# Kernel optimization log

Hardware: AMD Instinct MI355X
Metric: run time of the kernel (lower is better)

Reference implementation:

```python
import jax, jax.numpy as jnp
import numpy as np

B, CIN, CMID, COUT, H, W = 4, 64, 128, 128, 128, 128
K = 9  # 3x3 taps
EPS = 1e-5


def conv3x3(x, w, b):
    # standard 3x3 conv, stride 1, pad 1, NCHW / OIHW
    y = jax.lax.conv_general_dilated(x, w, (1, 1), ((1, 1), (1, 1)),
                                     dimension_numbers=('NCHW', 'OIHW', 'NCHW'))
    return y + b[None, :, None, None]


def deform_conv3x3(x, offset, w, b):
    # torchvision DeformConv2d semantics (v1, no mask), kernel 3, pad 1, stride 1.
    # offset: [B, 2*K, H, W] with per-tap (dy, dx) pairs.
    Bn, C, Hn, Wn = x.shape
    off = offset.reshape(Bn, K, 2, Hn, Wn)
    off_y, off_x = off[:, :, 0], off[:, :, 1]          # [B,K,H,W]
    ky = (jnp.arange(K) // 3).astype(x.dtype)          # tap row 0..2
    kx = (jnp.arange(K) % 3).astype(x.dtype)           # tap col 0..2
    # sampling positions: p = out_pos - pad + tap + offset
    py = jnp.arange(Hn, dtype=x.dtype)[None, None, :, None] - 1.0 + ky[None, :, None, None] + off_y
    px = jnp.arange(Wn, dtype=x.dtype)[None, None, None, :] - 1.0 + kx[None, :, None, None] + off_x
    y0 = jnp.floor(py); x0 = jnp.floor(px)
    wy1 = py - y0; wx1 = px - x0                       # bilinear fractions
    y0i = y0.astype(jnp.int32); x0i = x0.astype(jnp.int32)
    xf = x.reshape(Bn, C, Hn * Wn)

    def gather(iy, ix):
        valid = ((iy >= 0) & (iy < Hn) & (ix >= 0) & (ix < Wn)).astype(x.dtype)
        idx = jnp.clip(iy, 0, Hn - 1) * Wn + jnp.clip(ix, 0, Wn - 1)  # [B,K,H,W]
        g = jax.vmap(lambda xb, ib: xb[:, ib])(xf, idx)               # [B,C,K,H,W]
        return g, valid

    g00, v00 = gather(y0i, x0i)
    g01, v01 = gather(y0i, x0i + 1)
    g10, v10 = gather(y0i + 1, x0i)
    g11, v11 = gather(y0i + 1, x0i + 1)

    def wmul(g, v, wgt):
        return g * (v * wgt)[:, None]                  # broadcast over channel dim

    sampled = (wmul(g00, v00, (1 - wy1) * (1 - wx1)) +
               wmul(g01, v01, (1 - wy1) * wx1) +
               wmul(g10, v10, wy1 * (1 - wx1)) +
               wmul(g11, v11, wy1 * wx1))              # [B,C,K,H,W]
    out = jnp.einsum('bckhw,ock->bohw', sampled, w.reshape(w.shape[0], C, K))
    return out + b[None, :, None, None]


def batchnorm_relu(x, gamma, beta):
    # training-mode BN: batch statistics over (N,H,W), biased variance
    mean = jnp.mean(x, axis=(0, 2, 3), keepdims=True)
    var = jnp.mean(jnp.square(x - mean), axis=(0, 2, 3), keepdims=True)
    y = (x - mean) * jax.lax.rsqrt(var + EPS)
    return jax.nn.relu(y * gamma[None, :, None, None] + beta[None, :, None, None])


def setup_inputs() -> dict:
    key = jax.random.key(0)
    ks = jax.random.split(key, 13)
    s = 0.05  # small weights keep offsets small / sampling mostly in-bounds
    return {
        'x': jax.random.normal(ks[0], (B, CIN, H, W), jnp.float32),
        'w_off1': jax.random.normal(ks[1], (2 * K, CIN, 3, 3), jnp.float32) * s,
        'b_off1': jnp.zeros((2 * K,), jnp.float32),
        'w1': jax.random.normal(ks[2], (CMID, CIN, 3, 3), jnp.float32) * s,
        'b1': jax.random.normal(ks[3], (CMID,), jnp.float32) * s,
        'g1': jnp.ones((CMID,), jnp.float32),
        'be1': jnp.zeros((CMID,), jnp.float32),
        'w_off2': jax.random.normal(ks[4], (2 * K, CMID, 3, 3), jnp.float32) * s,
        'b_off2': jnp.zeros((2 * K,), jnp.float32),
        'w2': jax.random.normal(ks[5], (COUT, CMID, 3, 3), jnp.float32) * s,
        'b2': jax.random.normal(ks[6], (COUT,), jnp.float32) * s,
        'g2': jnp.ones((COUT,), jnp.float32),
        'be2': jnp.zeros((COUT,), jnp.float32),
    }


def reference(x, w_off1, b_off1, w1, b1, g1, be1, w_off2, b_off2, w2, b2, g2, be2):
    offset1 = conv3x3(x, w_off1, b_off1)
    out = deform_conv3x3(x, offset1, w1, b1)
    out = batchnorm_relu(out, g1, be1)
    offset2 = conv3x3(out, w_off2, b_off2)
    out = deform_conv3x3(out, offset2, w2, b2)
    out = batchnorm_relu(out, g2, be2)
    return out
```

## Files before the change

kernel.cpp:

```cpp
#include <hip/hip_runtime.h>
#include <hip/hip_bf16.h>

#define BB 4
#define H_ 128
#define W_ 128
#define HWP 16384
#define KOFF 18

typedef short short8 __attribute__((ext_vector_type(8)));
typedef float floatx4 __attribute__((ext_vector_type(4)));

#define WS_AB   16
#define WS_CVT  288
#define CVT_TOTAL 4447396
#define WS_WF1  4447744
#define WS_WF2  4484608
#define WS_XT   4558336
#define WS_Y1   7835136
#define WS_Y1T  16223744
#define WS_XTL  18320896
#define WS_WFO1 20418048
#define WS_WFO2 20436480
#define WS_PART 21600000
#define WS_Y2   WS_Y1

#define R_X     0
#define R_WOFF1 4194304
#define R_BOFF1 4204672
#define R_W1    4204690
#define R_B1    4278418
#define R_G1    4278546
#define R_BE1   4278674
#define R_WOFF2 4278802
#define R_BOFF2 4299538
#define R_W2    4299556
#define R_B2    4447012
#define R_G2    4447140
#define R_BE2   4447268

struct SrcPtrs { const void* p[13]; };

__device__ inline short f2bf(float f) {
    __hip_bfloat16 h = __float2bfloat16(f);
    return *reinterpret_cast<short*>(&h);
}
__device__ inline float bf2f(unsigned short u) {
    return __uint_as_float(((unsigned int)u) << 16);
}
__device__ inline float bfu_lo(unsigned int u) { return __uint_as_float(u << 16); }
__device__ inline float bfu_hi(unsigned int u) { return __uint_as_float(u & 0xFFFF0000u); }
__device__ inline float rl_f(float v, int i) {
    return __int_as_float(__builtin_amdgcn_readlane(__float_as_int(v), i));
}

__global__ void probe_dtype_k(const unsigned int* __restrict__ g1, int* __restrict__ flag) {
    if (threadIdx.x == 0 && blockIdx.x == 0) {
        flag[0] = ((g1[0] & 0xFFFFu) != 0u) ? 1 : 0;
    }
}

__global__ __launch_bounds__(256) void convert_inputs_k(SrcPtrs sp, float* __restrict__ dst,
                                                        const int* __restrict__ flag, int total) {
    int i = blockIdx.x * 256 + threadIdx.x;
    if (i >= total) return;
    constexpr int prefix[13] = {0, R_WOFF1, R_BOFF1, R_W1, R_B1, R_G1, R_BE1,
                                R_WOFF2, R_BOFF2, R_W2, R_B2, R_G2, R_BE2};
    const void* src = sp.p[0];
    int base = 0;
#pragma unroll
    for (int q = 1; q < 13; ++q) {
        if (i >= prefix[q]) { src = sp.p[q]; base = prefix[q]; }
    }
    int local = i - base;
    float v;
    if (flag[0] != 0) {
        v = bf2f(((const unsigned short*)src)[local]);
    } else {
        v = ((const float*)src)[local];
    }
    dst[i] = v;
}

template <int CIN>
__global__ __launch_bounds__(256) void wf_build_k(const float* __restrict__ w, short* __restrict__ wf) {
    constexpr int KSTEPS = CIN * 9 / 32;
    int idx = blockIdx.x * 256 + threadIdx.x;
    int j    = idx & 7;
    int lane = (idx >> 3) & 63;
    int rem  = idx >> 9;
    int ks   = rem % KSTEPS;
    int ct   = rem / KSTEPS;
    int co = ct * 16 + (lane & 15);
    int k  = ks * 32 + (lane >> 4) * 8 + j;
    int ci = k & (CIN - 1);
    int kk = k / CIN;
    wf[idx] = f2bf(w[(co * CIN + ci) * 9 + kk]);
}

template <int CIN>
__global__ __launch_bounds__(256) void wf_off_build_k(const float* __restrict__ w, short* __restrict__ wf) {
    constexpr int KSTEPS = CIN * 9 / 32;
    int idx = blockIdx.x * 256 + threadIdx.x;
    int j    = idx & 7;
    int lane = (idx >> 3) & 63;
    int rem  = idx >> 9;
    int ks   = rem % KSTEPS;
    int cc   = rem / KSTEPS;
    int sel  = cc >> 1;
    int co = (cc & 1) * 16 + (lane & 15);
    int k  = ks * 32 + (lane >> 4) * 8 + j;
    int ci = k & (CIN - 1);
    int kk = k / CIN;
    float v = (co < KOFF) ? w[(co * CIN + ci) * 9 + kk] : 0.f;
    short hi = f2bf(v);
    wf[idx] = sel ? f2bf(v - bf2f((unsigned short)hi)) : hi;
}

__global__ __launch_bounds__(256) void xt_build_k(const float* __restrict__ x,
                                                  unsigned short* __restrict__ xt,
                                                  unsigned short* __restrict__ xtl) {
    __shared__ __align__(4) short s_t[64 * 66];
    __shared__ __align__(4) short s_tl[64 * 66];
    int bi  = blockIdx.x;
    int hw0 = (bi & 255) * 64;
    int b   = bi >> 8;
    int t   = threadIdx.x;
    int hwp = t & 63;
#pragma unroll
    for (int it = 0; it < 16; ++it) {
        int c = it * 4 + (t >> 6);
        float v = x[((long)(b * 64 + c) << 14) + hw0 + hwp];
        short hi = f2bf(v);
        s_t[hwp * 66 + c]  = hi;
        s_tl[hwp * 66 + c] = f2bf(v - bf2f((unsigned short)hi));
    }
    __syncthreads();
#pragma unroll
    for (int it = 0; it < 8; ++it) {
        int i  = it * 256 + t;
        int c2 = (i & 31) * 2;
        int hw2 = i >> 5;
        long da = ((long)((b << 14) + hw0 + hw2)) * 64 + c2;
        *(int*)&xt[da]  = *(const int*)&s_t[hw2 * 66 + c2];
        *(int*)&xtl[da] = *(const int*)&s_tl[hw2 * 66 + c2];
    }
}

__device__ inline int conv_tpk(int h, int w0, int lane, int wv) {
    int tpk = 0;
    if (lane < 36) {
        int r = wv + 8 * lane;
        int p = r & 31;
        int k = r >> 5;
        int y = h - 1 + k / 3;
        int x = w0 + p - 1 + (k % 3);
        int valid = (y >= 0 && y < H_ && x >= 0 && x < W_) ? 1 : 0;
        int yc = min(max(y, 0), H_ - 1), xc = min(max(x, 0), W_ - 1);
        tpk = (yc * W_ + xc) | (valid << 16);
    }
    return tpk;
}

template <int NJ>
__device__ inline void conv_load64(const unsigned short* __restrict__ xb, unsigned int* ub,
                                   int half, int li, int tpk, int J0) {
#pragma unroll
    for (int j = 0; j < NJ; ++j) {
        int jj = J0 + j;
        int pkA = __builtin_amdgcn_readlane(tpk, 2 * jj);
        int pkB = __builtin_amdgcn_readlane(tpk, 2 * jj + 1);
        int pk = half ? pkB : pkA;
        unsigned int u = *(const unsigned int*)(xb + (pk & 0xFFFF) * 64 + 2 * li);
        ub[j] = (pk >> 16) ? u : 0u;
    }
}
template <int NJ, int PADc>
__device__ inline void conv_store64(short* __restrict__ s_samp, const unsigned int* ub,
                                    int half, int li, int wv, int J0) {
#pragma unroll
    for (int j = 0; j < NJ; ++j) {
        int jj = J0 + j;
        int r = wv + 8 * (half ? (2 * jj + 1) : (2 * jj));
        *(unsigned int*)&s_samp[(r & 31) * PADc + (r >> 5) * 64 + 2 * li] = ub[j];
    }
}
template <int I0, int NJ>
__device__ inline void conv_load128(const unsigned short* __restrict__ xb, unsigned int* ub,
                                    int lane, int tpk) {
#pragma unroll
    for (int j = 0; j < NJ; ++j) {
        int pk = __builtin_amdgcn_readlane(tpk, I0 + j);
        unsigned int u = *(const unsigned int*)(xb + (pk & 0xFFFF) * 128 + 2 * lane);
        ub[j] = (pk >> 16) ? u : 0u;
    }
}
template <int I0, int NJ, int KKB, int PADc>
__device__ inline void conv_store128(short* __restrict__ s_samp, const unsigned int* ub,
                                     int wv, int lane) {
#pragma unroll
    for (int j = 0; j < NJ; ++j) {
        int r = wv + 8 * (I0 + j);
        *(unsigned int*)&s_samp[(r & 31) * PADc + ((r >> 5) - KKB) * 128 + 2 * lane] = ub[j];
    }
}

__device__ inline void build_table2_lds(const float* __restrict__ s_off,
                                        int h, int w0, int lane, int wv,
                                        int& tpk, float& tw0, float& tw1, float& tw2, float& tw3) {
    tpk = 0; tw0 = tw1 = tw2 = tw3 = 0.f;
    if (lane < 36) {
        int r = wv + 8 * lane;
        int p = r & 31;
        int k = r >> 5;
        int wpix = w0 + p;
        float oy = s_off[(2 * k) * 32 + p];
        float ox = s_off[(2 * k + 1) * 32 + p];
        float py = (float)(h - 1 + (k / 3)) + oy;
        float px = (float)(wpix - 1 + (k % 3)) + ox;
        float fy = floorf(py), fx = floorf(px);
        float wy = py - fy, wx = px - fx;
        int y0 = (int)fy, x0 = (int)fx;
        int y1 = y0 + 1, x1 = x0 + 1;
        bool vy0 = (y0 >= 0) && (y0 < H_);
        bool vy1 = (y1 >= 0) && (y1 < H_);
        bool vx0 = (x0 >= 0) && (x0 < W_);
        bool vx1 = (x1 >= 0) && (x1 < W_);
        float wy0 = 1.f - wy, wx0 = 1.f - wx;
        tw0 = (vy0 && vx0) ? wy0 * wx0 : 0.f;
        tw1 = (vy0 && vx1) ? wy0 * wx  : 0.f;
        tw2 = (vy1 && vx0) ? wy  * wx0 : 0.f;
        tw3 = (vy1 && vx1) ? wy  * wx  : 0.f;
        int iy0 = min(max(y0, 0), H_ - 1), iy1 = min(max(y1, 0), H_ - 1);
        int ix0 = min(max(x0, 0), W_ - 1), ix1 = min(max(x1, 0), W_ - 1);
        int dx = ix1 - ix0;
        int dy = iy1 - iy0;
        tpk = (iy0 * W_ + ix0) | (dx << 14) | (dy << 15);
    }
}

template <int NB>
__device__ inline void gather_batch128v2(const unsigned short* __restrict__ xb, short* __restrict__ s_samp,
                                         int i0, int kkbase, int wv, int lane,
                                         int tpk, float tw0, float tw1, float tw2, float tw3) {
    constexpr int PADc = 648;
    uint4 ub[NB];
#pragma unroll
    for (int j = 0; j < NB; ++j) {
        int pk = __builtin_amdgcn_readlane(tpk, i0 + j);
        const unsigned short* b00 = xb + (pk & 0x3FFF) * 128;
        const unsigned short* b01 = b00 + ((pk >> 14) & 1) * 128;
        const unsigned short* b10 = b00 + ((pk >> 15) & 1) * (W_ * 128);
        const unsigned short* b11 = b01 + ((pk >> 15) & 1) * (W_ * 128);
        ub[j].x = *(const unsigned int*)(b00 + 2 * lane);
        ub[j].y = *(const unsigned int*)(b01 + 2 * lane);
        ub[j].z = *(const unsigned int*)(b10 + 2 * lane);
        ub[j].w = *(const unsigned int*)(b11 + 2 * lane);
    }
#pragma unroll
    for (int j = 0; j < NB; ++j) {
        int i = i0 + j;
        int r = wv + 8 * i;
        float w00 = rl_f(tw0, i), w01 = rl_f(tw1, i), w10 = rl_f(tw2, i), w11 = rl_f(tw3, i);
        float vlo = w00 * bfu_lo(ub[j].x) + w01 * bfu_lo(ub[j].y)
                  + w10 * bfu_lo(ub[j].z) + w11 * bfu_lo(ub[j].w);
        float vhi = w00 * bfu_hi(ub[j].x) + w01 * bfu_hi(ub[j].y)
                  + w10 * bfu_hi(ub[j].z) + w11 * bfu_hi(ub[j].w);
        __hip_bfloat162 h2 = __float22bfloat162_rn(make_float2(vlo, vhi));
        *(unsigned int*)&s_samp[(r & 31) * PADc + ((r >> 5) - kkbase) * 128 + 2 * lane] =
            *reinterpret_cast<unsigned int*>(&h2);
    }
}

template <int NBP>
__device__ inline void gather_batch64v2(const unsigned short* __restrict__ xb, short* __restrict__ s_samp,
                                        int i0, int wv, int half, int li,
                                        int tpk, float tw0, float tw1, float tw2, float tw3) {
    constexpr int PADc = 584;
    uint4 ub[NBP];
#pragma unroll
    for (int j = 0; j < NBP; ++j) {
        int iA = i0 + 2 * j, iB = iA + 1;
        int pkA = __builtin_amdgcn_readlane(tpk, iA);
        int pkB = __builtin_amdgcn_readlane(tpk, iB);
        int pk = half ? pkB : pkA;
        const unsigned short* b00 = xb + (pk & 0x3FFF) * 64;
        const unsigned short* b01 = b00 + ((pk >> 14) & 1) * 64;
        const unsigned short* b10 = b00 + ((pk >> 15) & 1) * (W_ * 64);
        const unsigned short* b11 = b01 + ((pk >> 15) & 1) * (W_ * 64);
        ub[j].x = *(const unsigned int*)(b00 + 2 * li);
        ub[j].y = *(const unsigned int*)(b01 + 2 * li);
        ub[j].z = *(const unsigned int*)(b10 + 2 * li);
        ub[j].w = *(const unsigned int*)(b11 + 2 * li);
    }
#pragma unroll
    for (int j = 0; j < NBP; ++j) {
        int iA = i0 + 2 * j, iB = iA + 1;
        float w00 = half ? rl_f(tw0, iB) : rl_f(tw0, iA);
        float w01 = half ? rl_f(tw1, iB) : rl_f(tw1, iA);
        float w10 = half ? rl_f(tw2, iB) : rl_f(tw2, iA);
        float w11 = half ? rl_f(tw3, iB) : rl_f(tw3, iA);
        float vlo = w00 * bfu_lo(ub[j].x) + w01 * bfu_lo(ub[j].y)
                  + w10 * bfu_lo(ub[j].z) + w11 * bfu_lo(ub[j].w);
        float vhi = w00 * bfu_hi(ub[j].x) + w01 * bfu_hi(ub[j].y)
                  + w10 * bfu_hi(ub[j].z) + w11 * bfu_hi(ub[j].w);
        __hip_bfloat162 h2 = __float22bfloat162_rn(make_float2(vlo, vhi));
        int r = wv + 8 * (half ? iB : iA);
        *(unsigned int*)&s_samp[(r & 31) * PADc + (r >> 5) * 64 + 2 * li] =
            *reinterpret_cast<unsigned int*>(&h2);
    }
}

__global__ __launch_bounds__(512, 4) void fused64_k(const unsigned short* __restrict__ xt,
                                                    const unsigned short* __restrict__ xtl,
                                                    const short* __restrict__ wfo,
                                                    const float* __restrict__ boff,
                                                    const short* __restrict__ wf,
                                                    const float* __restrict__ bias,
                                                    float* __restrict__ out) {
    constexpr int KSTEPS = 18;
    constexpr int PADc = 584;
    __shared__ __align__(16) short s_samp[32 * PADc];
    __shared__ float s_off[KOFF * 32];
    float* s_redf = (float*)s_samp;

    int bi = blockIdx.x;
    int w0 = (bi & 3) * 32;
    int h  = (bi >> 2) & 127;
    int b  = bi >> 9;
    int t  = threadIdx.x;
    int lane = t & 63;
    int wv   = t >> 6;

    const unsigned short* xbh = xt  + (long)b * HWP * 64;
    const unsigned short* xbl = xtl + (long)b * HWP * 64;
    int half = lane >> 5, li = lane & 31;
    int p_   = lane & 15;
    int quad = lane >> 4;

    {
        int tpkc = conv_tpk(h, w0, lane, wv);
        int ct  = wv & 1;
        int ksl = wv >> 1;
        floatx4 acc0, acc1;
#pragma unroll
        for (int r = 0; r < 4; ++r) {
            int co = ct * 16 + quad * 4 + r;
            float bv = (ksl == 0 && co < KOFF) ? boff[co] : 0.f;
            acc0[r] = bv;
            acc1[r] = bv;
        }

        {
            unsigned int ubA[16];
            conv_load64<16>(xbh, ubA, half, li, tpkc, 0);
            conv_store64<16, PADc>(s_samp, ubA, half, li, wv, 0);
        }
        __syncthreads();
        unsigned int ubC[2];
        conv_load64<2>(xbh, ubC, half, li, tpkc, 16);
#pragma unroll
        for (int ki = 0; ki < 4; ++ki) {
            int ks = ksl * 4 + ki;
            short8 b0 = *(const short8*)&s_samp[p_ * PADc + ks * 32 + quad * 8];
            short8 b1 = *(const short8*)&s_samp[(16 + p_) * PADc + ks * 32 + quad * 8];
            short8 ah = *(const short8*)&wfo[(((long)ct * KSTEPS + ks) * 64 + lane) * 8];
            short8 al = *(const short8*)&wfo[(((long)(2 + ct) * KSTEPS + ks) * 64 + lane) * 8];
            acc0 = __builtin_amdgcn_mfma_f32_16x16x32_bf16(ah, b0, acc0, 0, 0, 0);
            acc0 = __builtin_amdgcn_mfma_f32_16x16x32_bf16(al, b0, acc0, 0, 0, 0);
            acc1 = __builtin_amdgcn_mfma_f32_16x16x32_bf16(ah, b1, acc1, 0, 0, 0);
            acc1 = __builtin_amdgcn_mfma_f32_16x16x32_bf16(al, b1, acc1, 0, 0, 0);
        }
        __syncthreads();
        conv_store64<2, PADc>(s_samp, ubC, half, li, wv, 16);
        __syncthreads();
        unsigned int ubA2[16];
        conv_load64<16>(xbl, ubA2, half, li, tpkc, 0);
        if (ksl < 2) {
            int ks = 16 + ksl;
            short8 b0 = *(const short8*)&s_samp[p_ * PADc + ks * 32 + quad * 8];
            short8 b1 = *(const short8*)&s_samp[(16 + p_) * PADc + ks * 32 + quad * 8];
            short8 ah = *(const short8*)&wfo[(((long)ct * KSTEPS + ks) * 64 + lane) * 8];
            short8 al = *(const short8*)&wfo[(((long)(2 + ct) * KSTEPS + ks) * 64 + lane) * 8];
            acc0 = __builtin_amdgcn_mfma_f32_16x16x32_bf16(ah, b0, acc0, 0, 0, 0);
            acc0 = __builtin_amdgcn_mfma_f32_16x16x32_bf16(al, b0, acc0, 0, 0, 0);
            acc1 = __builtin_amdgcn_mfma_f32_16x16x32_bf16(ah, b1, acc1, 0, 0, 0);
            acc1 = __builtin_amdgcn_mfma_f32_16x16x32_bf16(al, b1, acc1, 0, 0, 0);
        }
        __syncthreads();
        conv_store64<16, PADc>(s_samp, ubA2, half, li, wv, 0);
        __syncthreads();
        conv_load64<2>(xbl, ubC, half, li, tpkc, 16);
#pragma unroll
        for (int ki = 0; ki < 4; ++ki) {
            int ks = ksl * 4 + ki;
            short8 b0 = *(const short8*)&s_samp[p_ * PADc + ks * 32 + quad * 8];
            short8 b1 = *(const short8*)&s_samp[(16 + p_) * PADc + ks * 32 + quad * 8];
            short8 ah = *(const short8*)&wfo[(((long)ct * KSTEPS + ks) * 64 + lane) * 8];
            acc0 = __builtin_amdgcn_mfma_f32_16x16x32_bf16(ah, b0, acc0, 0, 0, 0);
            acc1 = __builtin_amdgcn_mfma_f32_16x16x32_bf16(ah, b1, acc1, 0, 0, 0);
        }
        __syncthreads();
        conv_store64<2, PADc>(s_samp, ubC, half, li, wv, 16);
        __syncthreads();
        if (ksl < 2) {
            int ks = 16 + ksl;
            short8 b0 = *(const short8*)&s_samp[p_ * PADc + ks * 32 + quad * 8];
            short8 b1 = *(const short8*)&s_samp[(16 + p_) * PADc + ks * 32 + quad * 8];
            short8 ah = *(const short8*)&wfo[(((long)ct * KSTEPS + ks) * 64 + lane) * 8];
            acc0 = __builtin_amdgcn_mfma_f32_16x16x32_bf16(ah, b0, acc0, 0, 0, 0);
            acc1 = __builtin_amdgcn_mfma_f32_16x16x32_bf16(ah, b1, acc1, 0, 0, 0);
        }

        __syncthreads();
        if (ksl != 0) {
#pragma unroll
            for (int r = 0; r < 4; ++r) {
                s_redf[(((ksl - 1) * 4 + ct * 2 + 0) * 256) + (quad * 4 + r) * 16 + p_] = acc0[r];
                s_redf[(((ksl - 1) * 4 + ct * 2 + 1) * 256) + (quad * 4 + r) * 16 + p_] = acc1[r];
            }
        }
        __syncthreads();
        if (ksl == 0) {
#pragma unroll
            for (int r = 0; r < 4; ++r) {
                int co = ct * 16 + quad * 4 + r;
                if (co < KOFF) {
                    float v0 = acc0[r], v1 = acc1[r];
#pragma unroll
                    for (int s = 1; s < 4; ++s) {
                        v0 += s_redf[(((s - 1) * 4 + ct * 2 + 0) * 256) + (quad * 4 + r) * 16 + p_];
                        v1 += s_redf[(((s - 1) * 4 + ct * 2 + 1) * 256) + (quad * 4 + r) * 16 + p_];
                    }
                    s_off[co * 32 + p_]      = v0;
                    s_off[co * 32 + 16 + p_] = v1;
                }
            }
        }
        __syncthreads();
    }

    int tpk; float tw0, tw1, tw2, tw3;
    build_table2_lds(s_off, h, w0, lane, wv, tpk, tw0, tw1, tw2, tw3);

    gather_batch64v2<6>(xbh, s_samp,  0, wv, half, li, tpk, tw0, tw1, tw2, tw3);
    gather_batch64v2<6>(xbh, s_samp, 12, wv, half, li, tpk, tw0, tw1, tw2, tw3);
    gather_batch64v2<6>(xbh, s_samp, 24, wv, half, li, tpk, tw0, tw1, tw2, tw3);
    __syncthreads();

    int ct = wv;
    floatx4 acc0, acc1;
#pragma unroll
    for (int r = 0; r < 4; ++r) {
        float bv = bias[ct * 16 + quad * 4 + r];
        acc0[r] = bv;
        acc1[r] = bv;
    }
#pragma unroll 3
    for (int ks = 0; ks < KSTEPS; ++ks) {
        short8 a  = *(const short8*)&wf[(((long)ct * KSTEPS + ks) * 64 + lane) * 8];
        short8 b0 = *(const short8*)&s_samp[p_ * PADc + ks * 32 + quad * 8];
        short8 b1 = *(const short8*)&s_samp[(16 + p_) * PADc + ks * 32 + quad * 8];
        acc0 = __builtin_amdgcn_mfma_f32_16x16x32_bf16(a, b0, acc0, 0, 0, 0);
        acc1 = __builtin_amdgcn_mfma_f32_16x16x32_bf16(a, b1, acc1, 0, 0, 0);
    }

    long ob = ((long)(b * 128) << 14) + (h << 7) + w0 + p_;
#pragma unroll
    for (int r = 0; r < 4; ++r) {
        long cpl = (long)(ct * 16 + quad * 4 + r) << 14;
        out[ob + cpl]      = acc0[r];
        out[ob + 16 + cpl] = acc1[r];
    }
}

__global__ __launch_bounds__(512, 4) void fused128_k(const unsigned short* __restrict__ xt,
                                                     const unsigned short* __restrict__ xtl,
                                                     const short* __restrict__ wfo,
                                                     const float* __restrict__ boff,
                                                     const short* __restrict__ wf,
                                                     const float* __restrict__ bias,
                                                     float* __restrict__ out) {
    constexpr int KSTEPS = 36;
    constexpr int PADc = 648;
    __shared__ __align__(16) short s_samp[32 * PADc];
    __shared__ float s_off[KOFF * 32];
    float* s_redf = (float*)s_samp;

    int bi = blockIdx.x;
    int w0 = (bi & 3) * 32;
    int h  = (bi >> 2) & 127;
    int b  = bi >> 9;
    int t  = threadIdx.x;
    int lane = t & 63;
    int wv   = t >> 6;

    const unsigned short* xbh = xt  + (long)b * HWP * 128;
    const unsigned short* xbl = xtl + (long)b * HWP * 128;
    int p_   = lane & 15;
    int quad = lane >> 4;

    {
        int tpkc = conv_tpk(h, w0, lane, wv);
        int ct  = wv & 1;
        int ksl = wv >> 1;
        floatx4 acc0, acc1;
#pragma unroll
        for (int r = 0; r < 4; ++r) {
            int co = ct * 16 + quad * 4 + r;
            float bv = (ksl == 0 && co < KOFF) ? boff[co] : 0.f;
            acc0[r] = bv;
            acc1[r] = bv;
        }

        unsigned int ubA[16], ubB[20];
        conv_load128<0, 16>(xbh, ubA, lane, tpkc);
        conv_store128<0, 16, 0, PADc>(s_samp, ubA, wv, lane);
        __syncthreads();
        conv_load128<16, 20>(xbh, ubB, lane, tpkc);
#pragma unroll
        for (int ki = 0; ki < 4; ++ki) {
            int ks = ksl * 4 + ki;
            short8 b0 = *(const short8*)&s_samp[p_ * PADc + ks * 32 + quad * 8];
            short8 b1 = *(const short8*)&s_samp[(16 + p_) * PADc + ks * 32 + quad * 8];
            short8 ah = *(const short8*)&wfo[(((long)ct * KSTEPS + ks) * 64 + lane) * 8];
            short8 al = *(const short8*)&wfo[(((long)(2 + ct) * KSTEPS + ks) * 64 + lane) * 8];
            acc0 = __builtin_amdgcn_mfma_f32_16x16x32_bf16(ah, b0, acc0, 0, 0, 0);
            acc0 = __builtin_amdgcn_mfma_f32_16x16x32_bf16(al, b0, acc0, 0, 0, 0);
            acc1 = __builtin_amdgcn_mfma_f32_16x16x32_bf16(ah, b1, acc1, 0, 0, 0);
            acc1 = __builtin_amdgcn_mfma_f32_16x16x32_bf16(al, b1, acc1, 0, 0, 0);
        }
        __syncthreads();
        conv_store128<16, 20, 4, PADc>(s_samp, ubB, wv, lane);
        __syncthreads();
        conv_load128<0, 16>(xbl, ubA, lane, tpkc);
#pragma unroll
        for (int ki = 0; ki < 5; ++ki) {
            int ks = 16 + ksl * 5 + ki;
            short8 b0 = *(const short8*)&s_samp[p_ * PADc + (ks - 16) * 32 + quad * 8];
            short8 b1 = *(const short8*)&s_samp[(16 + p_) * PADc + (ks - 16) * 32 + quad * 8];
            short8 ah = *(const short8*)&wfo[(((long)ct * KSTEPS + ks) * 64 + lane) * 8];
            short8 al = *(const short8*)&wfo[(((long)(2 + ct) * KSTEPS + ks) * 64 + lane) * 8];
            acc0 = __builtin_amdgcn_mfma_f32_16x16x32_bf16(ah, b0, acc0, 0, 0, 0);
            acc0 = __builtin_amdgcn_mfma_f32_16x16x32_bf16(al, b0, acc0, 0, 0, 0);
            acc1 = __builtin_amdgcn_mfma_f32_16x16x32_bf16(ah, b1, acc1, 0, 0, 0);
            acc1 = __builtin_amdgcn_mfma_f32_16x16x32_bf16(al, b1, acc1, 0, 0, 0);
        }
        __syncthreads();
        conv_store128<0, 16, 0, PADc>(s_samp, ubA, wv, lane);
        __syncthreads();
        conv_load128<16, 20>(xbl, ubB, lane, tpkc);
#pragma unroll
        for (int ki = 0; ki < 4; ++ki) {
            int ks = ksl * 4 + ki;
            short8 b0 = *(const short8*)&s_samp[p_ * PADc + ks * 32 + quad * 8];
            short8 b1 = *(const short8*)&s_samp[(16 + p_) * PADc + ks * 32 + quad * 8];
            short8 ah = *(const short8*)&wfo[(((long)ct * KSTEPS + ks) * 64 + lane) * 8];
            acc0 = __builtin_amdgcn_mfma_f32_16x16x32_bf16(ah, b0, acc0, 0, 0, 0);
            acc1 = __builtin_amdgcn_mfma_f32_16x16x32_bf16(ah, b1, acc1, 0, 0, 0);
        }
        __syncthreads();
        conv_store128<16, 20, 4, PADc>(s_samp, ubB, wv, lane);
        __syncthreads();
#pragma unroll
        for (int ki = 0; ki < 5; ++ki) {
            int ks = 16 + ksl * 5 + ki;
            short8 b0 = *(const short8*)&s_samp[p_ * PADc + (ks - 16) * 32 + quad * 8];
            short8 b1 = *(const short8*)&s_samp[(16 + p_) * PADc + (ks - 16) * 32 + quad * 8];
            short8 ah = *(const short8*)&wfo[(((long)ct * KSTEPS + ks) * 64 + lane) * 8];
            acc0 = __builtin_amdgcn_mfma_f32_16x16x32_bf16(ah, b0, acc0, 0, 0, 0);
            acc1 = __builtin_amdgcn_mfma_f32_16x16x32_bf16(ah, b1, acc1, 0, 0, 0);
        }

        __syncthreads();
        if (ksl != 0) {
#pragma unroll
            for (int r = 0; r < 4; ++r) {
                s_redf[(((ksl - 1) * 4 + ct * 2 + 0) * 256) + (quad * 4 + r) * 16 + p_] = acc0[r];
                s_redf[(((ksl - 1) * 4 + ct * 2 + 1) * 256) + (quad * 4 + r) * 16 + p_] = acc1[r];
            }
        }
        __syncthreads();
        if (ksl == 0) {
#pragma unroll
            for (int r = 0; r < 4; ++r) {
                int co = ct * 16 + quad * 4 + r;
                if (co < KOFF) {
                    float v0 = acc0[r], v1 = acc1[r];
#pragma unroll
                    for (int s = 1; s < 4; ++s) {
                        v0 += s_redf[(((s - 1) * 4 + ct * 2 + 0) * 256) + (quad * 4 + r) * 16 + p_];
                        v1 += s_redf[(((s - 1) * 4 + ct * 2 + 1) * 256) + (quad * 4 + r) * 16 + p_];
                    }
                    s_off[co * 32 + p_]      = v0;
                    s_off[co * 32 + 16 + p_] = v1;
                }
            }
        }
        __syncthreads();
    }

    int tpk; float tw0, tw1, tw2, tw3;
    build_table2_lds(s_off, h, w0, lane, wv, tpk, tw0, tw1, tw2, tw3);

    int ct = wv;
    floatx4 acc0, acc1;
#pragma unroll
    for (int r = 0; r < 4; ++r) {
        float bv = bias[ct * 16 + quad * 4 + r];
        acc0[r] = bv;
        acc1[r] = bv;
    }

    gather_batch128v2<8>(xbh, s_samp, 0, 0, wv, lane, tpk, tw0, tw1, tw2, tw3);
    gather_batch128v2<8>(xbh, s_samp, 8, 0, wv, lane, tpk, tw0, tw1, tw2, tw3);
    __syncthreads();
#pragma unroll 4
    for (int ks = 0; ks < 16; ++ks) {
        short8 a  = *(const short8*)&wf[(((long)ct * KSTEPS + ks) * 64 + lane) * 8];
        short8 b0 = *(const short8*)&s_samp[p_ * PADc + ks * 32 + quad * 8];
        short8 b1 = *(const short8*)&s_samp[(16 + p_) * PADc + ks * 32 + quad * 8];
        acc0 = __builtin_amdgcn_mfma_f32_16x16x32_bf16(a, b0, acc0, 0, 0, 0);
        acc1 = __builtin_amdgcn_mfma_f32_16x16x32_bf16(a, b1, acc1, 0, 0, 0);
    }
    __syncthreads();

    gather_batch128v2<5>(xbh, s_samp, 16, 4, wv, lane, tpk, tw0, tw1, tw2, tw3);
    gather_batch128v2<5>(xbh, s_samp, 21, 4, wv, lane, tpk, tw0, tw1, tw2, tw3);
    gather_batch128v2<5>(xbh, s_samp, 26, 4, wv, lane, tpk, tw0, tw1, tw2, tw3);
    gather_batch128v2<5>(xbh, s_samp, 31, 4, wv, lane, tpk, tw0, tw1, tw2, tw3);
    __syncthreads();
#pragma unroll 4
    for (int ks = 16; ks < KSTEPS; ++ks) {
        short8 a  = *(const short8*)&wf[(((long)ct * KSTEPS + ks) * 64 + lane) * 8];
        short8 b0 = *(const short8*)&s_samp[p_ * PADc + (ks - 16) * 32 + quad * 8];
        short8 b1 = *(const short8*)&s_samp[(16 + p_) * PADc + (ks - 16) * 32 + quad * 8];
        acc0 = __builtin_amdgcn_mfma_f32_16x16x32_bf16(a, b0, acc0, 0, 0, 0);
        acc1 = __builtin_amdgcn_mfma_f32_16x16x32_bf16(a, b1, acc1, 0, 0, 0);
    }

    long ob = ((long)(b * 128) << 14) + (h << 7) + w0 + p_;
#pragma unroll
    for (int r = 0; r < 4; ++r) {
        long cpl = (long)(ct * 16 + quad * 4 + r) << 14;
        out[ob + cpl]      = acc0[r];
        out[ob + 16 + cpl] = acc1[r];
    }
}

__global__ __launch_bounds__(256) void bn_stats_part_k(const float* __restrict__ y, float* __restrict__ part) {
    int bi = blockIdx.x;
    int c = bi & 127;
    int b = bi >> 7;
    int t = threadIdx.x;
    const float4* p4 = (const float4*)(y + ((long)(b * 128 + c) << 14));
    float sum = 0.f, ss = 0.f;
#pragma unroll
    for (int i = 0; i < 16; ++i) {
        float4 v = p4[t + 256 * i];
        sum += v.x + v.y + v.z + v.w;
        ss  += v.x * v.x + v.y * v.y + v.z * v.z + v.w * v.w;
    }
#pragma unroll
    for (int o = 32; o > 0; o >>= 1) { sum += __shfl_down(sum, o); ss += __shfl_down(ss, o); }
    __shared__ float s1[4], s2[4];
    int wave = t >> 6;
    if ((t & 63) == 0) { s1[wave] = sum; s2[wave] = ss; }
    __syncthreads();
    if (t == 0) {
        part[bi]       = s1[0] + s1[1] + s1[2] + s1[3];
        part[512 + bi] = s2[0] + s2[1] + s2[2] + s2[3];
    }
}

__global__ __launch_bounds__(256) void bn_apply_dual_k(const float* __restrict__ y, const float* __restrict__ part,
                                                       const float* __restrict__ g, const float* __restrict__ be,
                                                       unsigned short* __restrict__ yt,
                                                       unsigned short* __restrict__ ytl) {
    __shared__ __align__(4) short s_t[64 * 134];
    __shared__ __align__(4) short s_tl[64 * 134];
    __shared__ float s_a[128], s_sh[128];
    int t = threadIdx.x;
    if (t < 128) {
        float sum = part[t] + part[128 + t] + part[256 + t] + part[384 + t];
        float ss  = part[512 + t] + part[640 + t] + part[768 + t] + part[896 + t];
        float mean = sum * (1.f / 65536.f);
        float var  = ss  * (1.f / 65536.f) - mean * mean;
        float inv  = rsqrtf(var + 1e-5f);
        float a = g[t] * inv;
        s_a[t]  = a;
        s_sh[t] = be[t] - mean * a;
    }
    __syncthreads();

    int bi  = blockIdx.x;
    int hw0 = (bi & 255) * 64;
    int b   = bi >> 8;
    int hwp = t & 63;
#pragma unroll 4
    for (int it = 0; it < 32; ++it) {
        int c = it * 4 + (t >> 6);
        float a = s_a[c], sh = s_sh[c];
        long addr = ((long)(b * 128 + c) << 14) + hw0 + hwp;
        float v = y[addr];
        v = fmaxf(v * a + sh, 0.f);
        short hi = f2bf(v);
        s_t[hwp * 134 + c]  = hi;
        s_tl[hwp * 134 + c] = f2bf(v - bf2f((unsigned short)hi));
    }
    __syncthreads();
#pragma unroll 4
    for (int it = 0; it < 16; ++it) {
        int i   = it * 256 + t;
        int c2  = (i & 63) * 2;
        int hw2 = i >> 6;
        long da = ((long)((b << 14) + hw0 + hw2)) * 128 + c2;
        *(int*)&yt[da]  = *(const int*)&s_t[hw2 * 134 + c2];
        *(int*)&ytl[da] = *(const int*)&s_tl[hw2 * 134 + c2];
    }
}

__global__ __launch_bounds__(256) void bn_apply_out_k(const float* __restrict__ y, const float* __restrict__ part,
                                                      const float* __restrict__ g, const float* __restrict__ be,
                                                      const int* __restrict__ flag, void* __restrict__ out, int total4) {
    __shared__ float s_a[128], s_sh[128];
    int t = threadIdx.x;
    if (t < 128) {
        float sum = part[t] + part[128 + t] + part[256 + t] + part[384 + t];
        float ss  = part[512 + t] + part[640 + t] + part[768 + t] + part[896 + t];
        float mean = sum * (1.f / 65536.f);
        float var  = ss  * (1.f / 65536.f) - mean * mean;
        float inv  = rsqrtf(var + 1e-5f);
        float a = g[t] * inv;
        s_a[t]  = a;
        s_sh[t] = be[t] - mean * a;
    }
    __syncthreads();

    int i = blockIdx.x * 256 + t;
    if (i >= total4) return;
    int c = (i >> 12) & 127;
    float a = s_a[c], sh = s_sh[c];
    float4 v = reinterpret_cast<const float4*>(y)[i];
    v.x = fmaxf(v.x * a + sh, 0.f);
    v.y = fmaxf(v.y * a + sh, 0.f);
    v.z = fmaxf(v.z * a + sh, 0.f);
    v.w = fmaxf(v.w * a + sh, 0.f);
    if (flag[0] != 0) {
        ushort4 u;
        u.x = (unsigned short)f2bf(v.x);
        u.y = (unsigned short)f2bf(v.y);
        u.z = (unsigned short)f2bf(v.z);
        u.w = (unsigned short)f2bf(v.w);
        reinterpret_cast<ushort4*>(out)[i] = u;
    } else {
        reinterpret_cast<float4*>(out)[i] = v;
    }
}

extern "C" void kernel_launch(void* const* d_in, const int* in_sizes, int n_in,
                              void* d_out, int out_size, void* d_ws, size_t ws_size,
                              hipStream_t stream) {
    float* ws   = (float*)d_ws;
    int*   flag = (int*)d_ws;
    float* cvt  = ws + WS_CVT;

    const float* X     = cvt + R_X;
    const float* Woff1 = cvt + R_WOFF1;
    const float* Boff1 = cvt + R_BOFF1;
    const float* W1f   = cvt + R_W1;
    const float* B1f   = cvt + R_B1;
    const float* G1    = cvt + R_G1;
    const float* Be1   = cvt + R_BE1;
    const float* Woff2 = cvt + R_WOFF2;
    const float* Boff2 = cvt + R_BOFF2;
    const float* W2f   = cvt + R_W2;
    const float* B2f   = cvt + R_B2;
    const float* G2    = cvt + R_G2;
    const float* Be2   = cvt + R_BE2;

    short* WF1  = (short*)(ws + WS_WF1);
    short* WF2  = (short*)(ws + WS_WF2);
    short* WFO1 = (short*)(ws + WS_WFO1);
    short* WFO2 = (short*)(ws + WS_WFO2);
    unsigned short* XT   = (unsigned short*)(ws + WS_XT);
    unsigned short* XTL  = (unsigned short*)(ws + WS_XTL);
    unsigned short* Y1T  = (unsigned short*)(ws + WS_Y1T);
    unsigned short* Y1TL = (unsigned short*)(ws + WS_CVT);
    float* PART = ws + WS_PART;
    float* Y1   = ws + WS_Y1;
    float* Y2   = ws + WS_Y2;

    SrcPtrs sp;
    for (int j = 0; j < 13; ++j) sp.p[j] = d_in[j];

    probe_dtype_k<<<1, 64, 0, stream>>>((const unsigned int*)d_in[5], flag);
    convert_inputs_k<<<(CVT_TOTAL + 255) / 256, 256, 0, stream>>>(sp, cvt, flag, CVT_TOTAL);
    wf_build_k<64><<<288, 256, 0, stream>>>(W1f, WF1);
    wf_build_k<128><<<576, 256, 0, stream>>>(W2f, WF2);
    wf_off_build_k<64><<<144, 256, 0, stream>>>(Woff1, WFO1);
    wf_off_build_k<128><<<288, 256, 0, stream>>>(Woff2, WFO2);
    xt_build_k<<<1024, 256, 0, stream>>>(X, XT, XTL);

    fused64_k<<<BB * 128 * 4, 512, 0, stream>>>(XT, XTL, WFO1, Boff1, WF1, B1f, Y1);
    bn_stats_part_k<<<512, 256, 0, stream>>>(Y1, PART);
    bn_apply_dual_k<<<1024, 256, 0, stream>>>(Y1, PART, G1, Be1, Y1T, Y1TL);

    fused128_k<<<BB * 128 * 4, 512, 0, stream>>>(Y1T, Y1TL, WFO2, Boff2, WF2, B2f, Y2);
    bn_stats_part_k<<<512, 256, 0, stream>>>(Y2, PART);
    bn_apply_out_k<<<(BB * 128 * HWP / 4 + 255) / 256, 256, 0, stream>>>(Y2, PART, G2, Be2, flag, d_out, BB * 128 * HWP / 4);
}
```

Measured before the change: 297.2 us.

## Shrink LDS sample tile by splitting K-steps into an extra tail phase

Reduces the padded shared-memory row width (PADc) to 520 in both fused kernels by staging the gathered/conv samples in three phases (16, 16, 4 ksteps for 128-ch; 16, 2 for 64-ch) instead of larger chunks. The tail K-steps are written at an offset base so the LDS buffer only needs to hold 16 ksteps. This cuts LDS per block, which may allow more resident blocks, at the cost of extra barriers and phases.

```diff
diff --git a/kernel.cpp b/kernel.cpp
--- a/kernel.cpp
+++ b/kernel.cpp
@@ -174,14 +174,14 @@
         ub[j] = (pk >> 16) ? u : 0u;
     }
 }
-template <int NJ, int PADc>
+template <int NJ, int PADc, int KKB>
 __device__ inline void conv_store64(short* __restrict__ s_samp, const unsigned int* ub,
                                     int half, int li, int wv, int J0) {
 #pragma unroll
     for (int j = 0; j < NJ; ++j) {
         int jj = J0 + j;
         int r = wv + 8 * (half ? (2 * jj + 1) : (2 * jj));
-        *(unsigned int*)&s_samp[(r & 31) * PADc + (r >> 5) * 64 + 2 * li] = ub[j];
+        *(unsigned int*)&s_samp[(r & 31) * PADc + ((r >> 5) - KKB) * 64 + 2 * li] = ub[j];
     }
 }
 template <int I0, int NJ>
@@ -242,7 +242,7 @@
 __device__ inline void gather_batch128v2(const unsigned short* __restrict__ xb, short* __restrict__ s_samp,
                                          int i0, int kkbase, int wv, int lane,
                                          int tpk, float tw0, float tw1, float tw2, float tw3) {
-    constexpr int PADc = 648;
+    constexpr int PADc = 520;
     uint4 ub[NB];
 #pragma unroll
     for (int j = 0; j < NB; ++j) {
@@ -273,9 +273,9 @@
 
 template <int NBP>
 __device__ inline void gather_batch64v2(const unsigned short* __restrict__ xb, short* __restrict__ s_samp,
-                                        int i0, int wv, int half, int li,
+                                        int i0, int kkbase, int wv, int half, int li,
                                         int tpk, float tw0, float tw1, float tw2, float tw3) {
-    constexpr int PADc = 584;
+    constexpr int PADc = 520;
     uint4 ub[NBP];
 #pragma unroll
     for (int j = 0; j < NBP; ++j) {
@@ -305,7 +305,7 @@
                   + w10 * bfu_hi(ub[j].z) + w11 * bfu_hi(ub[j].w);
         __hip_bfloat162 h2 = __float22bfloat162_rn(make_float2(vlo, vhi));
         int r = wv + 8 * (half ? iB : iA);
-        *(unsigned int*)&s_samp[(r & 31) * PADc + (r >> 5) * 64 + 2 * li] =
+        *(unsigned int*)&s_samp[(r & 31) * PADc + ((r >> 5) - kkbase) * 64 + 2 * li] =
             *reinterpret_cast<unsigned int*>(&h2);
     }
 }
@@ -318,7 +318,7 @@
                                                     const float* __restrict__ bias,
                                                     float* __restrict__ out) {
     constexpr int KSTEPS = 18;
-    constexpr int PADc = 584;
+    constexpr int PADc = 520;
     __shared__ __align__(16) short s_samp[32 * PADc];
     __shared__ float s_off[KOFF * 32];
     float* s_redf = (float*)s_samp;
@@ -353,7 +353,7 @@
         {
             unsigned int ubA[16];
             conv_load64<16>(xbh, ubA, half, li, tpkc, 0);
-            conv_store64<16, PADc>(s_samp, ubA, half, li, wv, 0);
+            conv_store64<16, PADc, 0>(s_samp, ubA, half, li, wv, 0);
         }
         __syncthreads();
         unsigned int ubC[2];
@@ -371,14 +371,14 @@
             acc1 = __builtin_amdgcn_mfma_f32_16x16x32_bf16(al, b1, acc1, 0, 0, 0);
         }
         __syncthreads();
-        conv_store64<2, PADc>(s_samp, ubC, half, li, wv, 16);
+        conv_store64<2, PADc, 8>(s_samp, ubC, half, li, wv, 16);
         __syncthreads();
         unsigned int ubA2[16];
         conv_load64<16>(xbl, ubA2, half, li, tpkc, 0);
         if (ksl < 2) {
             int ks = 16 + ksl;
-            short8 b0 = *(const short8*)&s_samp[p_ * PADc + ks * 32 + quad * 8];
-            short8 b1 = *(const short8*)&s_samp[(16 + p_) * PADc + ks * 32 + quad * 8];
+            short8 b0 = *(const short8*)&s_samp[p_ * PADc + (ks - 16) * 32 + quad * 8];
+            short8 b1 = *(const short8*)&s_samp[(16 + p_) * PADc + (ks - 16) * 32 + quad * 8];
             short8 ah = *(const short8*)&wfo[(((long)ct * KSTEPS + ks) * 64 + lane) * 8];
             short8 al = *(const short8*)&wfo[(((long)(2 + ct) * KSTEPS + ks) * 64 + lane) * 8];
             acc0 = __builtin_amdgcn_mfma_f32_16x16x32_bf16(ah, b0, acc0, 0, 0, 0);
@@ -387,7 +387,7 @@
             acc1 = __builtin_amdgcn_mfma_f32_16x16x32_bf16(al, b1, acc1, 0, 0, 0);
         }
         __syncthreads();
-        conv_store64<16, PADc>(s_samp, ubA2, half, li, wv, 0);
+        conv_store64<16, PADc, 0>(s_samp, ubA2, half, li, wv, 0);
         __syncthreads();
         conv_load64<2>(xbl, ubC, half, li, tpkc, 16);
 #pragma unroll
@@ -400,12 +400,12 @@
             acc1 = __builtin_amdgcn_mfma_f32_16x16x32_bf16(ah, b1, acc1, 0, 0, 0);
         }
         __syncthreads();
-        conv_store64<2, PADc>(s_samp, ubC, half, li, wv, 16);
+        conv_store64<2, PADc, 8>(s_samp, ubC, half, li, wv, 16);
         __syncthreads();
         if (ksl < 2) {
             int ks = 16 + ksl;
-            short8 b0 = *(const short8*)&s_samp[p_ * PADc + ks * 32 + quad * 8];
-            short8 b1 = *(const short8*)&s_samp[(16 + p_) * PADc + ks * 32 + quad * 8];
+            short8 b0 = *(const short8*)&s_samp[p_ * PADc + (ks - 16) * 32 + quad * 8];
+            short8 b1 = *(const short8*)&s_samp[(16 + p_) * PADc + (ks - 16) * 32 + quad * 8];
             short8 ah = *(const short8*)&wfo[(((long)ct * KSTEPS + ks) * 64 + lane) * 8];
             acc0 = __builtin_amdgcn_mfma_f32_16x16x32_bf16(ah, b0, acc0, 0, 0, 0);
             acc1 = __builtin_amdgcn_mfma_f32_16x16x32_bf16(ah, b1, acc1, 0, 0, 0);
@@ -442,11 +442,6 @@
     int tpk; float tw0, tw1, tw2, tw3;
     build_table2_lds(s_off, h, w0, lane, wv, tpk, tw0, tw1, tw2, tw3);
 
-    gather_batch64v2<6>(xbh, s_samp,  0, wv, half, li, tpk, tw0, tw1, tw2, tw3);
-    gather_batch64v2<6>(xbh, s_samp, 12, wv, half, li, tpk, tw0, tw1, tw2, tw3);
-    gather_batch64v2<6>(xbh, s_samp, 24, wv, half, li, tpk, tw0, tw1, tw2, tw3);
-    __syncthreads();
-
     int ct = wv;
     floatx4 acc0, acc1;
 #pragma unroll
@@ -455,11 +450,27 @@
         acc0[r] = bv;
         acc1[r] = bv;
     }
-#pragma unroll 3
-    for (int ks = 0; ks < KSTEPS; ++ks) {
+
+    gather_batch64v2<8>(xbh, s_samp,  0, 0, wv, half, li, tpk, tw0, tw1, tw2, tw3);
+    gather_batch64v2<8>(xbh, s_samp, 16, 0, wv, half, li, tpk, tw0, tw1, tw2, tw3);
+    __syncthreads();
+#pragma unroll 4
+    for (int ks = 0; ks < 16; ++ks) {
         short8 a  = *(const short8*)&wf[(((long)ct * KSTEPS + ks) * 64 + lane) * 8];
         short8 b0 = *(const short8*)&s_samp[p_ * PADc + ks * 32 + quad * 8];
         short8 b1 = *(const short8*)&s_samp[(16 + p_) * PADc + ks * 32 + quad * 8];
+        acc0 = __builtin_amdgcn_mfma_f32_16x16x32_bf16(a, b0, acc0, 0, 0, 0);
+        acc1 = __builtin_amdgcn_mfma_f32_16x16x32_bf16(a, b1, acc1, 0, 0, 0);
+    }
+    __syncthreads();
+
+    gather_batch64v2<2>(xbh, s_samp, 32, 8, wv, half, li, tpk, tw0, tw1, tw2, tw3);
+    __syncthreads();
+#pragma unroll
+    for (int ks = 16; ks < KSTEPS; ++ks) {
+        short8 a  = *(const short8*)&wf[(((long)ct * KSTEPS + ks) * 64 + lane) * 8];
+        short8 b0 = *(const short8*)&s_samp[p_ * PADc + (ks - 16) * 32 + quad * 8];
+        short8 b1 = *(const short8*)&s_samp[(16 + p_) * PADc + (ks - 16) * 32 + quad * 8];
         acc0 = __builtin_amdgcn_mfma_f32_16x16x32_bf16(a, b0, acc0, 0, 0, 0);
         acc1 = __builtin_amdgcn_mfma_f32_16x16x32_bf16(a, b1, acc1, 0, 0, 0);
     }
@@ -481,7 +492,7 @@
                                                      const float* __restrict__ bias,
                                                      float* __restrict__ out) {
     constexpr int KSTEPS = 36;
-    constexpr int PADc = 648;
+    constexpr int PADc = 520;
     __shared__ __align__(16) short s_samp[32 * PADc];
     __shared__ float s_off[KOFF * 32];
     float* s_redf = (float*)s_samp;
@@ -512,11 +523,11 @@
             acc1[r] = bv;
         }
 
-        unsigned int ubA[16], ubB[20];
+        unsigned int ubA[16], ubB[16], ubC[4];
         conv_load128<0, 16>(xbh, ubA, lane, tpkc);
         conv_store128<0, 16, 0, PADc>(s_samp, ubA, wv, lane);
         __syncthreads();
-        conv_load128<16, 20>(xbh, ubB, lane, tpkc);
+        conv_load128<16, 16>(xbh, ubB, lane, tpkc);
 #pragma unroll
         for (int ki = 0; ki < 4; ++ki) {
             int ks = ksl * 4 + ki;
@@ -530,12 +541,12 @@
             acc1 = __builtin_amdgcn_mfma_f32_16x16x32_bf16(al, b1, acc1, 0, 0, 0);
         }
         __syncthreads();
-        conv_store128<16, 20, 4, PADc>(s_samp, ubB, wv, lane);
-        __syncthreads();
-        conv_load128<0, 16>(xbl, ubA, lane, tpkc);
-#pragma unroll
-        for (int ki = 0; ki < 5; ++ki) {
-            int ks = 16 + ksl * 5 + ki;
+        conv_store128<16, 16, 4, PADc>(s_samp, ubB, wv, lane);
+        __syncthreads();
+        conv_load128<32, 4>(xbh, ubC, lane, tpkc);
+#pragma unroll
+        for (int ki = 0; ki < 4; ++ki) {
+            int ks = 16 + ksl * 4 + ki;
             short8 b0 = *(const short8*)&s_samp[p_ * PADc + (ks - 16) * 32 + quad * 8];
             short8 b1 = *(const short8*)&s_samp[(16 + p_) * PADc + (ks - 16) * 32 + quad * 8];
             short8 ah = *(const short8*)&wfo[(((long)ct * KSTEPS + ks) * 64 + lane) * 8];
@@ -546,9 +557,24 @@
             acc1 = __builtin_amdgcn_mfma_f32_16x16x32_bf16(al, b1, acc1, 0, 0, 0);
         }
         __syncthreads();
+        conv_store128<32, 4, 8, PADc>(s_samp, ubC, wv, lane);
+        __syncthreads();
+        conv_load128<0, 16>(xbl, ubA, lane, tpkc);
+        {
+            int ks = 32 + ksl;
+            short8 b0 = *(const short8*)&s_samp[p_ * PADc + (ks - 32) * 32 + quad * 8];
+            short8 b1 = *(const short8*)&s_samp[(16 + p_) * PADc + (ks - 32) * 32 + quad * 8];
+            short8 ah = *(const short8*)&wfo[(((long)ct * KSTEPS + ks) * 64 + lane) * 8];
+            short8 al = *(const short8*)&wfo[(((long)(2 + ct) * KSTEPS + ks) * 64 + lane) * 8];
+            acc0 = __builtin_amdgcn_mfma_f32_16x16x32_bf16(ah, b0, acc0, 0, 0, 0);
+            acc0 = __builtin_amdgcn_mfma_f32_16x16x32_bf16(al, b0, acc0, 0, 0, 0);
+            acc1 = __builtin_amdgcn_mfma_f32_16x16x32_bf16(ah, b1, acc1, 0, 0, 0);
+            acc1 = __builtin_amdgcn_mfma_f32_16x16x32_bf16(al, b1, acc1, 0, 0, 0);
+        }
+        __syncthreads();
         conv_store128<0, 16, 0, PADc>(s_samp, ubA, wv, lane);
         __syncthreads();
-        conv_load128<16, 20>(xbl, ubB, lane, tpkc);
+        conv_load128<16, 16>(xbl, ubB, lane, tpkc);
 #pragma unroll
         for (int ki = 0; ki < 4; ++ki) {
             int ks = ksl * 4 + ki;
@@ -559,13 +585,25 @@
             acc1 = __builtin_amdgcn_mfma_f32_16x16x32_bf16(ah, b1, acc1, 0, 0, 0);
         }
         __syncthreads();
-        conv_store128<16, 20, 4, PADc>(s_samp, ubB, wv, lane);
-        __syncthreads();
-#pragma unroll
-        for (int ki = 0; ki < 5; ++ki) {
-            int ks = 16 + ksl * 5 + ki;
+        conv_store128<16, 16, 4, PADc>(s_samp, ubB, wv, lane);
+        __syncthreads();
+        conv_load128<32, 4>(xbl, ubC, lane, tpkc);
+#pragma unroll
+        for (int ki = 0; ki < 4; ++ki) {
+            int ks = 16 + ksl * 4 + ki;
             short8 b0 = *(const short8*)&s_samp[p_ * PADc + (ks - 16) * 32 + quad * 8];
             short8 b1 = *(const short8*)&s_samp[(16 + p_) * PADc + (ks - 16) * 32 + quad * 8];
+            short8 ah = *(const short8*)&wfo[(((long)ct * KSTEPS + ks) * 64 + lane) * 8];
+            acc0 = __builtin_amdgcn_mfma_f32_16x16x32_bf16(ah, b0, acc0, 0, 0, 0);
+            acc1 = __builtin_amdgcn_mfma_f32_16x16x32_bf16(ah, b1, acc1, 0, 0, 0);
+        }
+        __syncthreads();
+        conv_store128<32, 4, 8, PADc>(s_samp, ubC, wv, lane);
+        __syncthreads();
+        {
+            int ks = 32 + ksl;
+            short8 b0 = *(const short8*)&s_samp[p_ * PADc + (ks - 32) * 32 + quad * 8];
+            short8 b1 = *(const short8*)&s_samp[(16 + p_) * PADc + (ks - 32) * 32 + quad * 8];
             short8 ah = *(const short8*)&wfo[(((long)ct * KSTEPS + ks) * 64 + lane) * 8];
             acc0 = __builtin_amdgcn_mfma_f32_16x16x32_bf16(ah, b0, acc0, 0, 0, 0);
             acc1 = __builtin_amdgcn_mfma_f32_16x16x32_bf16(ah, b1, acc1, 0, 0, 0);
@@ -624,16 +662,26 @@
     }
     __syncthreads();
 
-    gather_batch128v2<5>(xbh, s_samp, 16, 4, wv, lane, tpk, tw0, tw1, tw2, tw3);
-    gather_batch128v2<5>(xbh, s_samp, 21, 4, wv, lane, tpk, tw0, tw1, tw2, tw3);
-    gather_batch128v2<5>(xbh, s_samp, 26, 4, wv, lane, tpk, tw0, tw1, tw2, tw3);
-    gather_batch128v2<5>(xbh, s_samp, 31, 4, wv, lane, tpk, tw0, tw1, tw2, tw3);
+    gather_batch128v2<8>(xbh, s_samp, 16, 4, wv, lane, tpk, tw0, tw1, tw2, tw3);
+    gather_batch128v2<8>(xbh, s_samp, 24, 4, wv, lane, tpk, tw0, tw1, tw2, tw3);
     __syncthreads();
 #pragma unroll 4
-    for (int ks = 16; ks < KSTEPS; ++ks) {
+    for (int ks = 16; ks < 32; ++ks) {
         short8 a  = *(const short8*)&wf[(((long)ct * KSTEPS + ks) * 64 + lane) * 8];
         short8 b0 = *(const short8*)&s_samp[p_ * PADc + (ks - 16) * 32 + quad * 8];
         short8 b1 = *(const short8*)&s_samp[(16 + p_) * PADc + (ks - 16) * 32 + quad * 8];
+        acc0 = __builtin_amdgcn_mfma_f32_16x16x32_bf16(a, b0, acc0, 0, 0, 0);
+        acc1 = __builtin_amdgcn_mfma_f32_16x16x32_bf16(a, b1, acc1, 0, 0, 0);
+    }
+    __syncthreads();
+
+    gather_batch128v2<4>(xbh, s_samp, 32, 8, wv, lane, tpk, tw0, tw1, tw2, tw3);
+    __syncthreads();
+#pragma unroll
+    for (int ks = 32; ks < KSTEPS; ++ks) {
+        short8 a  = *(const short8*)&wf[(((long)ct * KSTEPS + ks) * 64 + lane) * 8];
+        short8 b0 = *(const short8*)&s_samp[p_ * PADc + (ks - 32) * 32 + quad * 8];
+        short8 b1 = *(const short8*)&s_samp[(16 + p_) * PADc + (ks - 32) * 32 + quad * 8];
         acc0 = __builtin_amdgcn_mfma_f32_16x16x32_bf16(a, b0, acc0, 0, 0, 0);
         acc1 = __builtin_amdgcn_mfma_f32_16x16x32_bf16(a, b1, acc1, 0, 0, 0);
     }
```

After: 299.9 us. Within noise of the previous version (+0.9%).
